# Kernel optimization log

Measured on AMD Instinct MI355X. Metric: run time of the kernel, lower is better.

The kernel has to match this reference:

```python
import jax, jax.numpy as jnp
import numpy as np
from jax import lax

B, N_SITES, FEAT, BOND, OUT = 2048, 128, 64, 32, 256
CORE_SCALE = 0.02  # keeps the 128-step matrix product finite


def setup_inputs() -> dict:
    key = jax.random.key(0)
    ks = jax.random.split(key, 6)
    return {
        "x": jax.random.normal(ks[0], (B, N_SITES, FEAT), dtype=jnp.float32),
        "cores": jax.random.normal(ks[1], (N_SITES, BOND, FEAT, BOND), dtype=jnp.float32) * CORE_SCALE,
        "start": jax.random.normal(ks[2], (1, BOND), dtype=jnp.float32),
        "end": jax.random.normal(ks[3], (BOND, 1), dtype=jnp.float32),
        "fc_w": jax.random.normal(ks[4], (OUT, 1), dtype=jnp.float32),
        "fc_b": jax.random.normal(ks[5], (OUT,), dtype=jnp.float32),
    }


def reference(x, cores, start, end, fc_w, fc_b):
    # x: [B, N, F]; cores: [N, D, F, D]; start: [1, D]; end: [D, 1]
    b = x.shape[0]
    res0 = jnp.broadcast_to(start, (b, start.shape[1]))  # [B, D]

    def step(res, site):
        xi, core = site  # xi: [B, F], core: [D, F, D]
        m = jnp.einsum('bf,dfr->bdr', xi, core)  # per-site transfer matrix [B, D, D]
        return jnp.einsum('bd,bdr->br', res, m), None

    res, _ = lax.scan(step, res0, (jnp.swapaxes(x, 0, 1), cores))
    val = res @ end  # [B, 1]
    return val @ fc_w.T + fc_b  # [B, OUT]
```

## Files before the change

kernel.cpp:

```cpp
#include <hip/hip_runtime.h>


#define NSITES 128
#define FEATD  64
#define BOND   32
#define OUTD   256
#define BT     16
#define SEGLEN 16
#define NSEG   (NSITES / SEGLEN)
#define NPAIR  (SEGLEN / 2)
#define NBT    (2048 / BT)

#define RSTRIDE 36
#define BSTRIDE 1164

typedef __attribute__((ext_vector_type(4))) float float4v;

__device__ __forceinline__ unsigned pk4_fp8(float a, float b, float c, float d) {
    int v = __builtin_amdgcn_cvt_pk_fp8_f32(a, b, 0, false);
    v = __builtin_amdgcn_cvt_pk_fp8_f32(c, d, v, true);
    return (unsigned)v;
}

__device__ __forceinline__ long ld8(const unsigned char* p) {
    unsigned lo = *(const unsigned*)p;
    unsigned hi = *(const unsigned*)(p + 4);
    return (long)(((unsigned long long)hi << 32) | (unsigned long long)lo);
}

__device__ __forceinline__ void af_load(long af[16], const unsigned char* __restrict__ core8,
                                        int n, int wave, int cl, int q) {
    const unsigned char* base = core8 + (size_t)n * (1024 * FEATD);
#pragma unroll
    for (int i = 0; i < 8; ++i) {
        const unsigned char* p = base + (size_t)((wave * 8 + i) * 16 + cl) * FEATD + q * 8;
        af[2 * i + 0] = *(const long*)p;
        af[2 * i + 1] = *(const long*)(p + 32);
    }
}

__device__ __forceinline__ long cvt_frag(float4v c0, float4v c1,
                                         int idxlo, int idxhi, int selhi) {
    const float s = 0.0625f;
    int d0 = (int)pk4_fp8(c0[0] * s, c0[1] * s, c0[2] * s, c0[3] * s);
    int d1 = (int)pk4_fp8(c1[0] * s, c1[1] * s, c1[2] * s, c1[3] * s);
    int l0 = __builtin_amdgcn_ds_bpermute(idxlo, d0);
    int l1 = __builtin_amdgcn_ds_bpermute(idxlo, d1);
    int h0 = __builtin_amdgcn_ds_bpermute(idxhi, d0);
    int h1 = __builtin_amdgcn_ds_bpermute(idxhi, d1);
    unsigned lo = (unsigned)(selhi ? l1 : l0);
    unsigned hi = (unsigned)(selhi ? h1 : h0);
    return (long)(((unsigned long long)hi << 32) | (unsigned long long)lo);
}

__global__ __launch_bounds__(256)
void prep_cores8(const float* __restrict__ cores, unsigned char* __restrict__ core8) {
    __shared__ float tile[FEATD][BOND + 4];
    const int nd = blockIdx.x;
    const int t  = threadIdx.x;
    const float* src = cores + (size_t)nd * (FEATD * BOND);
    {
        int base = t * 8;
        int f = base >> 5, r0 = base & 31;
        float4 v0 = *(const float4*)(src + base);
        float4 v1 = *(const float4*)(src + base + 4);
        tile[f][r0 + 0] = v0.x; tile[f][r0 + 1] = v0.y;
        tile[f][r0 + 2] = v0.z; tile[f][r0 + 3] = v0.w;
        tile[f][r0 + 4] = v1.x; tile[f][r0 + 5] = v1.y;
        tile[f][r0 + 6] = v1.z; tile[f][r0 + 7] = v1.w;
    }
    __syncthreads();
    const int r = t >> 3, f0 = (t & 7) * 8;
    const float s = 16.0f;
    unsigned lo = pk4_fp8(tile[f0 + 0][r] * s, tile[f0 + 1][r] * s,
                          tile[f0 + 2][r] * s, tile[f0 + 3][r] * s);
    unsigned hi = pk4_fp8(tile[f0 + 4][r] * s, tile[f0 + 5][r] * s,
                          tile[f0 + 6][r] * s, tile[f0 + 7][r] * s);
    uint2 w; w.x = lo; w.y = hi;
    *(uint2*)(core8 + ((size_t)nd * BOND + r) * FEATD + f0) = w;
}

__global__ __launch_bounds__(512, 4)
void mps_seg(const float* __restrict__ x, const unsigned char* __restrict__ core8,
             unsigned char* __restrict__ Pout) {
    __shared__ __align__(16) unsigned char MA[BT * BSTRIDE];
    __shared__ __align__(16) unsigned char MB[BT * BSTRIDE];
    __shared__ __align__(16) unsigned char NT[BT * BSTRIDE];
    __shared__ __align__(16) unsigned char XS[2][2][BT * 72];

    const int t    = threadIdx.x;
    const int wave = t >> 6;
    const int lane = t & 63;
    const int cl   = lane & 15;
    const int q    = lane >> 4;
    const int bt   = blockIdx.x;
    const int seg  = blockIdx.y;
    const int b0   = bt * BT;
    const int xb   = t >> 5, xf = (t & 31) * 2;

    const int idxlo = (cl + 16 * ((2 * q) & 3)) << 2;
    const int idxhi = (cl + 16 * ((2 * q + 1) & 3)) << 2;
    const int selhi = q >> 1;

    long ps[2][2];
#pragma unroll
    for (int J = 0; J < 2; ++J) {
        int row = J * 16 + cl;
        int jj  = row - 8 * q;
        long v  = (jj >= 0 && jj < 8) ? (long)(0x58ULL << (8 * jj)) : 0L;
        ps[0][J] = v;
        ps[1][J] = v;
    }

    const int n0 = seg * SEGLEN;

    const float* xptr = x + ((size_t)(b0 + xb) * NSITES + n0) * FEATD + xf;
    float2 xa  = *(const float2*)xptr;
    float2 xbv = *(const float2*)(xptr + FEATD);
    {
        int v0 = __builtin_amdgcn_cvt_pk_fp8_f32(xa.x, xa.y, 0, false);
        *(unsigned short*)&XS[0][0][xb * 72 + xf] = (unsigned short)(v0 & 0xffff);
        int v1 = __builtin_amdgcn_cvt_pk_fp8_f32(xbv.x, xbv.y, 0, false);
        *(unsigned short*)&XS[0][1][xb * 72 + xf] = (unsigned short)(v1 & 0xffff);
    }
    long afa[16];
    af_load(afa, core8, n0, wave, cl, q);
    __syncthreads();

    for (int j = 0; j < NPAIR; ++j) {
        const int n = n0 + 2 * j;

        {
            const unsigned char* xsA = &XS[j & 1][0][0];
            const unsigned char* xsB = &XS[j & 1][1][0];
            long bxa0 = *(const long*)(xsA + cl * 72 + q * 8);
            long bxa1 = *(const long*)(xsA + cl * 72 + 32 + q * 8);
            long bxb0 = *(const long*)(xsB + cl * 72 + q * 8);
            long bxb1 = *(const long*)(xsB + cl * 72 + 32 + q * 8);

            long afb[16];
            af_load(afb, core8, n + 1, wave, cl, q);

            float4v acc[8];
#pragma unroll
            for (int i = 0; i < 8; ++i) {
                float4v z = {0.f, 0.f, 0.f, 0.f};
                z = __builtin_amdgcn_mfma_f32_16x16x32_fp8_fp8(afa[2 * i + 0], bxa0, z, 0, 0, 0);
                acc[i] = __builtin_amdgcn_mfma_f32_16x16x32_fp8_fp8(afa[2 * i + 1], bxa1, z, 0, 0, 0);
            }
#pragma unroll
            for (int i = 0; i < 8; ++i) {
                unsigned w = pk4_fp8(acc[i][0], acc[i][1], acc[i][2], acc[i][3]);
                *(unsigned*)&MA[cl * BSTRIDE + (wave * 4 + (i >> 1)) * RSTRIDE
                                + (i & 1) * 16 + q * 4] = w;
            }

            if (j + 1 < NPAIR) {
                const float* xp = x + ((size_t)(b0 + xb) * NSITES + n + 2) * FEATD + xf;
                xa  = *(const float2*)xp;
                xbv = *(const float2*)(xp + FEATD);
            }

            float4v accb[8];
#pragma unroll
            for (int i = 0; i < 8; ++i) {
                float4v z = {0.f, 0.f, 0.f, 0.f};
                z = __builtin_amdgcn_mfma_f32_16x16x32_fp8_fp8(afb[2 * i + 0], bxb0, z, 0, 0, 0);
                accb[i] = __builtin_amdgcn_mfma_f32_16x16x32_fp8_fp8(afb[2 * i + 1], bxb1, z, 0, 0, 0);
            }
#pragma unroll
            for (int p = 0; p < 2; ++p)
#pragma unroll
                for (int g = 0; g < 4; ++g) {
                    unsigned w = pk4_fp8(accb[0 + p][g], accb[2 + p][g],
                                         accb[4 + p][g], accb[6 + p][g]);
                    *(unsigned*)&MB[cl * BSTRIDE + (16 * p + 4 * q + g) * RSTRIDE
                                    + wave * 4] = w;
                }
        }
        __syncthreads();

        {
            if (j + 1 < NPAIR) {
                int v0 = __builtin_amdgcn_cvt_pk_fp8_f32(xa.x, xa.y, 0, false);
                *(unsigned short*)&XS[(j + 1) & 1][0][xb * 72 + xf] = (unsigned short)(v0 & 0xffff);
                int v1 = __builtin_amdgcn_cvt_pk_fp8_f32(xbv.x, xbv.y, 0, false);
                *(unsigned short*)&XS[(j + 1) & 1][1][xb * 72 + xf] = (unsigned short)(v1 & 0xffff);
                af_load(afa, core8, n + 2, wave, cl, q);
            }

#pragma unroll
            for (int bi = 0; bi < 2; ++bi) {
                const int bb = wave * 2 + bi;
                const unsigned char* mab = &MA[bb * BSTRIDE];
                const unsigned char* mbb = &MB[bb * BSTRIDE];
                long pa0 = ld8(mab + cl * RSTRIDE + q * 8);
                long pa1 = ld8(mab + (16 + cl) * RSTRIDE + q * 8);
                long pb0 = ld8(mbb + cl * RSTRIDE + q * 8);
                long pb1 = ld8(mbb + (16 + cl) * RSTRIDE + q * 8);
                float4v z00 = {0.f, 0.f, 0.f, 0.f}, z01 = {0.f, 0.f, 0.f, 0.f};
                float4v z10 = {0.f, 0.f, 0.f, 0.f}, z11 = {0.f, 0.f, 0.f, 0.f};
                z00 = __builtin_amdgcn_mfma_f32_16x16x32_fp8_fp8(pa0, pb0, z00, 0, 0, 0);
                z01 = __builtin_amdgcn_mfma_f32_16x16x32_fp8_fp8(pa0, pb1, z01, 0, 0, 0);
                z10 = __builtin_amdgcn_mfma_f32_16x16x32_fp8_fp8(pa1, pb0, z10, 0, 0, 0);
                z11 = __builtin_amdgcn_mfma_f32_16x16x32_fp8_fp8(pa1, pb1, z11, 0, 0, 0);
                unsigned char* nb = &NT[bb * BSTRIDE];
                const float s = 0.0625f;
                unsigned w00 = pk4_fp8(z00[0] * s, z00[1] * s, z00[2] * s, z00[3] * s);
                unsigned w01 = pk4_fp8(z01[0] * s, z01[1] * s, z01[2] * s, z01[3] * s);
                unsigned w10 = pk4_fp8(z10[0] * s, z10[1] * s, z10[2] * s, z10[3] * s);
                unsigned w11 = pk4_fp8(z11[0] * s, z11[1] * s, z11[2] * s, z11[3] * s);
                *(unsigned*)&nb[(0 * 16 + cl) * RSTRIDE + 0 * 16 + q * 4] = w00;
                *(unsigned*)&nb[(1 * 16 + cl) * RSTRIDE + 0 * 16 + q * 4] = w01;
                *(unsigned*)&nb[(0 * 16 + cl) * RSTRIDE + 1 * 16 + q * 4] = w10;
                *(unsigned*)&nb[(1 * 16 + cl) * RSTRIDE + 1 * 16 + q * 4] = w11;
            }

#pragma unroll
            for (int bi = 0; bi < 2; ++bi) {
                const int bb = wave * 2 + bi;
                const unsigned char* nb = &NT[bb * BSTRIDE];
                long ca0 = ld8(nb + cl * RSTRIDE + q * 8);
                long ca1 = ld8(nb + (16 + cl) * RSTRIDE + q * 8);
                float4v c00 = {0.f, 0.f, 0.f, 0.f}, c01 = {0.f, 0.f, 0.f, 0.f};
                float4v c10 = {0.f, 0.f, 0.f, 0.f}, c11 = {0.f, 0.f, 0.f, 0.f};
                c00 = __builtin_amdgcn_mfma_f32_16x16x32_fp8_fp8(ca0, ps[bi][0], c00, 0, 0, 0);
                c01 = __builtin_amdgcn_mfma_f32_16x16x32_fp8_fp8(ca0, ps[bi][1], c01, 0, 0, 0);
                c10 = __builtin_amdgcn_mfma_f32_16x16x32_fp8_fp8(ca1, ps[bi][0], c10, 0, 0, 0);
                c11 = __builtin_amdgcn_mfma_f32_16x16x32_fp8_fp8(ca1, ps[bi][1], c11, 0, 0, 0);
                ps[bi][0] = cvt_frag(c00, c10, idxlo, idxhi, selhi);
                ps[bi][1] = cvt_frag(c01, c11, idxlo, idxhi, selhi);
            }
        }
        __syncthreads();
    }

#pragma unroll
    for (int bi = 0; bi < 2; ++bi) {
        const int bb = wave * 2 + bi;
        unsigned char* gp = Pout + ((size_t)seg * 2048 + b0 + bb) * 1024;
#pragma unroll
        for (int J = 0; J < 2; ++J)
            *(long*)(gp + (J * 16 + cl) * 32 + q * 8) = ps[bi][J];
    }
}

__global__ __launch_bounds__(256)
void combine(const unsigned char* __restrict__ Pout, const float* __restrict__ startv,
             const float* __restrict__ endv, const float* __restrict__ fc_w,
             const float* __restrict__ fc_b, float* __restrict__ out) {
    __shared__ __align__(16) unsigned char st[8 * 1024];
    __shared__ float resA[8][33], resB[8][33];
    __shared__ float val[8];
    const int t  = threadIdx.x;
    const int b0 = blockIdx.x * 8;
    const int bb = t >> 5, r = t & 31;

    resA[bb][r] = startv[r];
    for (int s = 0; s < NSEG; ++s) {
        {
            const uint4* g = (const uint4*)(Pout + ((size_t)s * 2048 + b0) * 1024 + (size_t)t * 32);
            uint4* p = (uint4*)&st[t * 32];
            p[0] = g[0];
            p[1] = g[1];
        }
        __syncthreads();
        const float* rin = (s & 1) ? &resB[bb][0] : &resA[bb][0];
        float* rout      = (s & 1) ? &resA[bb][0] : &resB[bb][0];
        float acc = 0.f;
#pragma unroll
        for (int d = 0; d < BOND; ++d) {
            int byte = st[bb * 1024 + d * 32 + r];
            acc += rin[d] * __builtin_amdgcn_cvt_f32_fp8(byte, 0);
        }
        rout[r] = acc * 0.0625f;
        __syncthreads();
    }
    float prod = resA[bb][r] * endv[r];
#pragma unroll
    for (int off = 16; off >= 1; off >>= 1) prod += __shfl_down(prod, off, 32);
    if (r == 0) val[bb] = prod;
    __syncthreads();

    const float v = val[t >> 5];
    const int j0 = (t & 31) * 8;
    const int ob = b0 + (t >> 5);
#pragma unroll
    for (int i = 0; i < 2; ++i) {
        int j = j0 + i * 4;
        float4 w4 = *(const float4*)(fc_w + j);
        float4 bbv = *(const float4*)(fc_b + j);
        float4 o;
        o.x = v * w4.x + bbv.x;
        o.y = v * w4.y + bbv.y;
        o.z = v * w4.z + bbv.z;
        o.w = v * w4.w + bbv.w;
        *(float4*)(out + (size_t)ob * OUTD + j) = o;
    }
}

extern "C" void kernel_launch(void* const* d_in, const int* in_sizes, int n_in,
                              void* d_out, int out_size, void* d_ws, size_t ws_size,
                              hipStream_t stream) {
    const float* x      = (const float*)d_in[0];
    const float* cores  = (const float*)d_in[1];
    const float* startv = (const float*)d_in[2];
    const float* endv   = (const float*)d_in[3];
    const float* fc_w   = (const float*)d_in[4];
    const float* fc_b   = (const float*)d_in[5];
    float* out = (float*)d_out;

    unsigned char* core8 = (unsigned char*)d_ws;
    unsigned char* Pout  = core8 + (size_t)NSITES * 1024 * FEATD;

    prep_cores8<<<NSITES * BOND, 256, 0, stream>>>(cores, core8);
    mps_seg<<<dim3(NBT, NSEG), 512, 0, stream>>>(x, core8, Pout);
    combine<<<2048 / 8, 256, 0, stream>>>(Pout, startv, endv, fc_w, fc_b, out);
}
```

Measured before the change: 245.0 us.

## Keep pair product in registers, raise occupancy, prefetch segments in combine

Several changes at once. The pair-product tile is converted directly from MFMA accumulators into fp8 fragments with cvt_frag instead of being written to and re-read from an extra LDS buffer, which frees that shared memory and lets launch bounds ask for 6 blocks per CU. The grid axes are swapped so segments of the same batch tile launch next to each other. MFMA bursts are bracketed by s_setprio, segment outputs are staged in LDS for coalesced 16-byte global stores, and combine loads all segment data up front. The direct conversion drops the 1/16 scale that the old NT write applied, so numerics may change unless cvt_frag compensates, and the higher occupancy target may force register spills.

```diff
diff --git a/kernel.cpp b/kernel.cpp
--- a/kernel.cpp
+++ b/kernel.cpp
@@ -80,12 +80,11 @@
     *(uint2*)(core8 + ((size_t)nd * BOND + r) * FEATD + f0) = w;
 }
 
-__global__ __launch_bounds__(512, 4)
+__global__ __launch_bounds__(512, 6)
 void mps_seg(const float* __restrict__ x, const unsigned char* __restrict__ core8,
              unsigned char* __restrict__ Pout) {
     __shared__ __align__(16) unsigned char MA[BT * BSTRIDE];
     __shared__ __align__(16) unsigned char MB[BT * BSTRIDE];
-    __shared__ __align__(16) unsigned char NT[BT * BSTRIDE];
     __shared__ __align__(16) unsigned char XS[2][2][BT * 72];
 
     const int t    = threadIdx.x;
@@ -93,8 +92,8 @@
     const int lane = t & 63;
     const int cl   = lane & 15;
     const int q    = lane >> 4;
-    const int bt   = blockIdx.x;
-    const int seg  = blockIdx.y;
+    const int seg  = blockIdx.x;
+    const int bt   = blockIdx.y;
     const int b0   = bt * BT;
     const int xb   = t >> 5, xf = (t & 31) * 2;
 
@@ -142,12 +141,14 @@
             af_load(afb, core8, n + 1, wave, cl, q);
 
             float4v acc[8];
+            __builtin_amdgcn_s_setprio(1);
 #pragma unroll
             for (int i = 0; i < 8; ++i) {
                 float4v z = {0.f, 0.f, 0.f, 0.f};
                 z = __builtin_amdgcn_mfma_f32_16x16x32_fp8_fp8(afa[2 * i + 0], bxa0, z, 0, 0, 0);
                 acc[i] = __builtin_amdgcn_mfma_f32_16x16x32_fp8_fp8(afa[2 * i + 1], bxa1, z, 0, 0, 0);
             }
+            __builtin_amdgcn_s_setprio(0);
 #pragma unroll
             for (int i = 0; i < 8; ++i) {
                 unsigned w = pk4_fp8(acc[i][0], acc[i][1], acc[i][2], acc[i][3]);
@@ -162,12 +163,14 @@
             }
 
             float4v accb[8];
+            __builtin_amdgcn_s_setprio(1);
 #pragma unroll
             for (int i = 0; i < 8; ++i) {
                 float4v z = {0.f, 0.f, 0.f, 0.f};
                 z = __builtin_amdgcn_mfma_f32_16x16x32_fp8_fp8(afb[2 * i + 0], bxb0, z, 0, 0, 0);
                 accb[i] = __builtin_amdgcn_mfma_f32_16x16x32_fp8_fp8(afb[2 * i + 1], bxb1, z, 0, 0, 0);
             }
+            __builtin_amdgcn_s_setprio(0);
 #pragma unroll
             for (int p = 0; p < 2; ++p)
 #pragma unroll
@@ -204,24 +207,8 @@
                 z01 = __builtin_amdgcn_mfma_f32_16x16x32_fp8_fp8(pa0, pb1, z01, 0, 0, 0);
                 z10 = __builtin_amdgcn_mfma_f32_16x16x32_fp8_fp8(pa1, pb0, z10, 0, 0, 0);
                 z11 = __builtin_amdgcn_mfma_f32_16x16x32_fp8_fp8(pa1, pb1, z11, 0, 0, 0);
-                unsigned char* nb = &NT[bb * BSTRIDE];
-                const float s = 0.0625f;
-                unsigned w00 = pk4_fp8(z00[0] * s, z00[1] * s, z00[2] * s, z00[3] * s);
-                unsigned w01 = pk4_fp8(z01[0] * s, z01[1] * s, z01[2] * s, z01[3] * s);
-                unsigned w10 = pk4_fp8(z10[0] * s, z10[1] * s, z10[2] * s, z10[3] * s);
-                unsigned w11 = pk4_fp8(z11[0] * s, z11[1] * s, z11[2] * s, z11[3] * s);
-                *(unsigned*)&nb[(0 * 16 + cl) * RSTRIDE + 0 * 16 + q * 4] = w00;
-                *(unsigned*)&nb[(1 * 16 + cl) * RSTRIDE + 0 * 16 + q * 4] = w01;
-                *(unsigned*)&nb[(0 * 16 + cl) * RSTRIDE + 1 * 16 + q * 4] = w10;
-                *(unsigned*)&nb[(1 * 16 + cl) * RSTRIDE + 1 * 16 + q * 4] = w11;
-            }
-
-#pragma unroll
-            for (int bi = 0; bi < 2; ++bi) {
-                const int bb = wave * 2 + bi;
-                const unsigned char* nb = &NT[bb * BSTRIDE];
-                long ca0 = ld8(nb + cl * RSTRIDE + q * 8);
-                long ca1 = ld8(nb + (16 + cl) * RSTRIDE + q * 8);
+                long ca0 = cvt_frag(z00, z10, idxlo, idxhi, selhi);
+                long ca1 = cvt_frag(z01, z11, idxlo, idxhi, selhi);
                 float4v c00 = {0.f, 0.f, 0.f, 0.f}, c01 = {0.f, 0.f, 0.f, 0.f};
                 float4v c10 = {0.f, 0.f, 0.f, 0.f}, c11 = {0.f, 0.f, 0.f, 0.f};
                 c00 = __builtin_amdgcn_mfma_f32_16x16x32_fp8_fp8(ca0, ps[bi][0], c00, 0, 0, 0);
@@ -238,10 +225,16 @@
 #pragma unroll
     for (int bi = 0; bi < 2; ++bi) {
         const int bb = wave * 2 + bi;
-        unsigned char* gp = Pout + ((size_t)seg * 2048 + b0 + bb) * 1024;
 #pragma unroll
         for (int J = 0; J < 2; ++J)
-            *(long*)(gp + (J * 16 + cl) * 32 + q * 8) = ps[bi][J];
+            *(long*)&MA[bb * 1024 + (J * 16 + cl) * 32 + q * 8] = ps[bi][J];
+    }
+    __syncthreads();
+    {
+        const uint4* p = (const uint4*)&MA[t * 32];
+        uint4* g = (uint4*)(Pout + ((size_t)seg * 2048 + b0) * 1024 + (size_t)t * 32);
+        g[0] = p[0];
+        g[1] = p[1];
     }
 }
 
@@ -256,13 +249,20 @@
     const int b0 = blockIdx.x * 8;
     const int bb = t >> 5, r = t & 31;
 
+    uint4 ga[NSEG][2];
+#pragma unroll
+    for (int s = 0; s < NSEG; ++s) {
+        const uint4* g = (const uint4*)(Pout + ((size_t)s * 2048 + b0) * 1024 + (size_t)t * 32);
+        ga[s][0] = g[0];
+        ga[s][1] = g[1];
+    }
+
     resA[bb][r] = startv[r];
     for (int s = 0; s < NSEG; ++s) {
         {
-            const uint4* g = (const uint4*)(Pout + ((size_t)s * 2048 + b0) * 1024 + (size_t)t * 32);
             uint4* p = (uint4*)&st[t * 32];
-            p[0] = g[0];
-            p[1] = g[1];
+            p[0] = ga[s][0];
+            p[1] = ga[s][1];
         }
         __syncthreads();
         const float* rin = (s & 1) ? &resB[bb][0] : &resA[bb][0];
@@ -314,6 +314,6 @@
     unsigned char* Pout  = core8 + (size_t)NSITES * 1024 * FEATD;
 
     prep_cores8<<<NSITES * BOND, 256, 0, stream>>>(cores, core8);
-    mps_seg<<<dim3(NBT, NSEG), 512, 0, stream>>>(x, core8, Pout);
+    mps_seg<<<dim3(NSEG, NBT), 512, 0, stream>>>(x, core8, Pout);
     combine<<<2048 / 8, 256, 0, stream>>>(Pout, startv, endv, fc_w, fc_b, out);
 }
```

After: 367.0 us. 1.5x slower.
